# Performance work log

Measured on AMD Instinct MI355X. Metric: run time of the kernel, lower is better.

The kernel has to match this reference:

```python
import jax, jax.numpy as jnp
import numpy as np
import math

B, H, N, D = 32, 8, 257, 64  # batch, heads, seq (256 patches + 1), head dim
DIM = H * D
PIX = 256  # 16*16 flattened mask pixels
EPS = 1e-5


def setup_inputs() -> dict:
    key = jax.random.key(0)
    k1, k2, k3 = jax.random.split(key, 3)
    x = jax.random.normal(k1, (B, N, DIM), dtype=jnp.float32)
    msk = jax.random.randint(k2, (B, 16, 16), 0, 128, dtype=jnp.int32)
    W_qkv = jax.random.normal(k3, (3 * DIM, DIM), dtype=jnp.float32) * (DIM ** -0.5)
    # past_kv initialized to identity per head (np.eye tiled in the torch forward)
    past_kv = jnp.broadcast_to(jnp.eye(D, dtype=jnp.float32), (B, H, D, D))
    gn_weight = jnp.ones((H,), dtype=jnp.float32)
    gn_bias = jnp.zeros((H,), dtype=jnp.float32)
    return {"x": x, "msk": msk, "W_qkv": W_qkv, "past_kv": past_kv,
            "gn_weight": gn_weight, "gn_bias": gn_bias}


def _build_mask(msk):
    # msk: [B,16,16] int; zeros replaced by pseudo-random ints in [1,128)
    noise = jax.random.randint(jax.random.key(42), msk.shape, 1, 128, dtype=jnp.int32)
    m = jnp.where(msk == 0, noise, msk).astype(jnp.float32)
    pix = m.reshape(B, PIX, 1)                       # [B,256,1]
    ip = pix @ jnp.swapaxes(pix, 1, 2)               # [B,256,256] outer product
    ip = ip / jnp.max(ip, axis=(1, 2), keepdims=True)
    dec0 = jnp.exp(-5.0 * jnp.linspace(0.0, 1.0, PIX))       # row [256]
    t = jnp.concatenate([jnp.broadcast_to(dec0[None, None, :], (B, 1, PIX)), ip], axis=1)  # [B,257,256]
    dec1 = jnp.exp(-5.0 * jnp.linspace(0.0, 1.0, N))         # col [257]
    t = jnp.concatenate([jnp.broadcast_to(dec1[None, :, None], (B, N, 1)), t], axis=2)     # [B,257,257]
    eye = jnp.eye(N, dtype=bool)
    t = jnp.where(eye, 1.0, t)   # fill_diagonal_(1)
    t = jnp.tril(t)
    return t[:, None, :, :]      # [B,1,N,N] broadcast over heads


def reference(x, msk, W_qkv, past_kv, gn_weight, gn_bias):
    scale = D ** -0.5  # decay_mask == chunk_decay == inner_decay == dim_heads**-0.5
    qkv = x @ W_qkv.T                                # [B,N,3*DIM]
    q, k, v = jnp.split(qkv, 3, axis=-1)
    def heads(t):
        return t.reshape(B, N, H, D).transpose(0, 2, 1, 3)  # b n (h d) -> b h n d
    q, k, v = heads(q), heads(k), heads(v)

    retention = jnp.einsum('bhnd,bhmd->bhnm', q, k) * scale
    weights_before = jax.nn.softmax(retention / math.sqrt(D), axis=-1)

    mask = _build_mask(msk)
    retention = retention * mask
    weights_after = jax.nn.softmax(retention / math.sqrt(D), axis=-1)

    inner_retention = jnp.einsum('bhnm,bhmd->bhnd', retention, v)
    cross_retention = jnp.einsum('bhnd,bhde->bhne', q, past_kv) * scale
    r = inner_retention + cross_retention            # [B,H,N,D]

    # GroupNorm(groups=H, channels=H): normalize each head over (N,D)
    mean = jnp.mean(r, axis=(2, 3), keepdims=True)
    var = jnp.mean((r - mean) ** 2, axis=(2, 3), keepdims=True)
    rn = (r - mean) / jnp.sqrt(var + EPS)
    rn = rn * gn_weight[None, :, None, None] + gn_bias[None, :, None, None]

    output = rn.transpose(0, 2, 1, 3).reshape(B, N, H * D)  # b h n d -> b n (h d)
    return (output, weights_before, weights_after)
```

## Files before the change

### kernel.cpp

```cpp
#include <hip/hip_runtime.h>
#include <stdint.h>

#define WB_OFF   4210688ull
#define WA_OFF   21119232ull

typedef short short8 __attribute__((ext_vector_type(8)));
typedef float floatx4 __attribute__((ext_vector_type(4)));
typedef __attribute__((address_space(1))) const unsigned int gu32;
typedef __attribute__((address_space(3))) unsigned int lu32;

__device__ __forceinline__ unsigned short f2bf(float f){
  union { float f; uint32_t u; } v; v.f = f;
  uint32_t u = v.u;
  uint32_t r = (u + 0x7FFFu + ((u >> 16) & 1u)) >> 16;
  return (unsigned short)r;
}

__device__ __forceinline__ void threefry(uint32_t k0, uint32_t k1, uint32_t c0, uint32_t c1,
                                         uint32_t& o0, uint32_t& o1){
  const uint32_t ks2 = k0 ^ k1 ^ 0x1BD11BDAu;
  uint32_t x0 = c0 + k0, x1 = c1 + k1;
#define TF_R4(a,b,c,d) \
  x0+=x1; x1=(x1<<(a))|(x1>>(32-(a))); x1^=x0; \
  x0+=x1; x1=(x1<<(b))|(x1>>(32-(b))); x1^=x0; \
  x0+=x1; x1=(x1<<(c))|(x1>>(32-(c))); x1^=x0; \
  x0+=x1; x1=(x1<<(d))|(x1>>(32-(d))); x1^=x0;
  TF_R4(13,15,26,6)  x0+=k1;  x1+=ks2+1u;
  TF_R4(17,29,16,24) x0+=ks2; x1+=k0+2u;
  TF_R4(13,15,26,6)  x0+=k0;  x1+=k1+3u;
  TF_R4(17,29,16,24) x0+=k1;  x1+=ks2+4u;
  TF_R4(13,15,26,6)  x0+=ks2; x1+=k0+5u;
#undef TF_R4
  o0 = x0; o1 = x1;
}

__global__ __launch_bounds__(256) void prep_kernel(const int* __restrict__ msk,
                                                   float* __restrict__ mnorm){
  const int b = blockIdx.x, p = threadIdx.x;
  const int i = b*256 + p;
  uint32_t A0, A1, B0, B1;
  threefry(0u, 42u, 0u, 0u, A0, A1);
  threefry(0u, 42u, 0u, 1u, B0, B1);
  uint32_t h0, h1, l0, l1;
  threefry(A0, A1, 0u, (uint32_t)i, h0, h1);
  threefry(B0, B1, 0u, (uint32_t)i, l0, l1);
  uint32_t hb = h0 ^ h1, lb = l0 ^ l1;
  uint32_t off = ((hb % 127u) * 16u + (lb % 127u)) % 127u;
  int mv = msk[i];
  float m = (mv == 0) ? (float)(1u + off) : (float)mv;
  __shared__ float sm[256];
  sm[p] = m; __syncthreads();
  for (int s = 128; s > 0; s >>= 1){
    if (p < s) sm[p] = fmaxf(sm[p], sm[p+s]);
    __syncthreads();
  }
  mnorm[i] = m / sm[0];
}

__global__ __launch_bounds__(256) void cvt_kernel(const float* __restrict__ x,
                                                  const float* __restrict__ w,
                                                  unsigned short* __restrict__ xb,
                                                  unsigned short* __restrict__ wb){
  int i = blockIdx.x*256 + threadIdx.x;
  if (i < 1052672){
    float4 v = ((const float4*)x)[i];
    ushort4 o; o.x=f2bf(v.x); o.y=f2bf(v.y); o.z=f2bf(v.z); o.w=f2bf(v.w);
    ((ushort4*)xb)[i] = o;
  } else if (i < 1249280){
    int j = i - 1052672;
    float4 v = ((const float4*)w)[j];
    ushort4 o; o.x=f2bf(v.x); o.y=f2bf(v.y); o.z=f2bf(v.z); o.w=f2bf(v.w);
    ((ushort4*)wb)[j] = o;
  }
}

__global__ __launch_bounds__(256) void qkv_gemm(const unsigned short* __restrict__ xb,
                                                const unsigned short* __restrict__ wb,
                                                unsigned short* __restrict__ qkv){
  __shared__ unsigned short sm2[128*64*2 + 128*8];
  unsigned short* al = sm2;
  unsigned short* bl = sm2 + 128*64;
  unsigned short* c_lds = sm2;
  const int bn = blockIdx.x, bm = blockIdx.y;
  const int tid = threadIdx.x;
  const int wave = tid >> 6, lane = tid & 63;
  const int l16 = lane & 15, lq = lane >> 4;
  const int wm = (wave & 1) * 64, wn = (wave >> 1) * 64;
  const int row0 = tid >> 3;
  const int ccg = ((tid & 7) ^ (row0 & 7)) * 8;
  const int sx = (l16 & 7);
  floatx4 acc[4][4] = {};
  for (int kk = 0; kk < 512; kk += 64){
    #pragma unroll
    for (int p = 0; p < 4; p++){
      int row = p*32 + row0;
      int gm = bm*128 + row; if (gm > 8223) gm = 8223;
      __builtin_amdgcn_global_load_lds((gu32*)&xb[(size_t)gm*512 + kk + ccg],
                                       (lu32*)&al[row*64 + (tid & 7)*8], 16, 0, 0);
      int gn = bn*128 + row;
      __builtin_amdgcn_global_load_lds((gu32*)&wb[(size_t)gn*512 + kk + ccg],
                                       (lu32*)&bl[row*64 + (tid & 7)*8], 16, 0, 0);
    }
    __syncthreads();
    #pragma unroll
    for (int ks = 0; ks < 2; ks++){
      short8 af[4], bf4[4];
      #pragma unroll
      for (int mi = 0; mi < 4; mi++){
        int ch = (ks*4 + lq) ^ sx;
        af[mi] = *(const short8*)&al[(wm + mi*16 + l16)*64 + ch*8];
      }
      #pragma unroll
      for (int ni = 0; ni < 4; ni++){
        int ch = (ks*4 + lq) ^ sx;
        bf4[ni] = *(const short8*)&bl[(wn + ni*16 + l16)*64 + ch*8];
      }
      #pragma unroll
      for (int mi = 0; mi < 4; mi++)
        #pragma unroll
        for (int ni = 0; ni < 4; ni++)
          acc[mi][ni] = __builtin_amdgcn_mfma_f32_16x16x32_bf16(af[mi], bf4[ni], acc[mi][ni], 0, 0, 0);
    }
    __syncthreads();
  }
  #pragma unroll
  for (int mi = 0; mi < 4; mi++)
    #pragma unroll
    for (int ni = 0; ni < 4; ni++)
      #pragma unroll
      for (int r = 0; r < 4; r++)
        c_lds[(wm + mi*16 + lq*4 + r)*136 + wn + ni*16 + l16] = f2bf(acc[mi][ni][r]);
  __syncthreads();
  for (int i = tid; i < 128*16; i += 256){
    int row = i >> 4, cc = (i & 15)*8;
    int gm = bm*128 + row;
    if (gm < 8224){
      ushort4 v0 = *(const ushort4*)&c_lds[row*136 + cc];
      ushort4 v1 = *(const ushort4*)&c_lds[row*136 + cc + 4];
      *(ushort4*)&qkv[(size_t)gm*1536 + bn*128 + cc] = v0;
      *(ushort4*)&qkv[(size_t)gm*1536 + bn*128 + cc + 4] = v1;
    }
  }
}

__global__ __launch_bounds__(256, 3) void retention_kernel(
    const unsigned short* __restrict__ qkv,
    const float* __restrict__ past_kv,
    const float* __restrict__ mnorm,
    float* __restrict__ out,
    float* __restrict__ partials){
  const int t  = blockIdx.x;
  const int bh = blockIdx.y;
  const int b = bh >> 3, h = bh & 7;
  const int tid = threadIdx.x;
  const int wave = tid >> 6, lane = tid & 63;
  const int l16 = lane & 15, lq = lane >> 4;
  const int rw = wave * 16;

  extern __shared__ unsigned char smem[];
  unsigned short* kl  = (unsigned short*)smem;
  unsigned short* vT  = (unsigned short*)smem;
  float* bufw         = (float*)(smem + wave*8224);
  unsigned short* pkl = (unsigned short*)(smem + 39168);
  unsigned short* plw = (unsigned short*)(smem + 39168 + wave*1280);
  float* mn  = (float*)(smem + 48384);
  float* red = (float*)(smem + 49408);

  {
    uint32_t* z = (uint32_t*)(kl + 257*72);
    for (int i = tid; i < 540; i += 256) z[i] = 0;
  }
  for (int c = tid; c < 257*16; c += 256){
    int row = c >> 4, c4 = (c & 15) * 4;
    ushort4 v = *(const ushort4*)&qkv[(size_t)(b*257 + row)*1536 + 512 + h*64 + c4];
    *(ushort4*)&kl[row*72 + c4] = v;
  }
  for (int c = tid; c < 64*16; c += 256){
    int d = c >> 4, e4 = (c & 15) * 4;
    float4 v = *(const float4*)&past_kv[(size_t)bh*4096 + d*64 + e4];
    pkl[(e4+0)*72 + d] = f2bf(0.125f * v.x);
    pkl[(e4+1)*72 + d] = f2bf(0.125f * v.y);
    pkl[(e4+2)*72 + d] = f2bf(0.125f * v.z);
    pkl[(e4+3)*72 + d] = f2bf(0.125f * v.w);
  }
  mn[tid] = mnorm[b*256 + tid];
  int giA = t*64 + rw + l16; if (giA > 256) giA = 256;
  short8 aq[2];
  aq[0] = *(const short8*)&qkv[(size_t)(b*257 + giA)*1536 + h*64 + lq*8];
  aq[1] = *(const short8*)&qkv[(size_t)(b*257 + giA)*1536 + h*64 + 32 + lq*8];
  __syncthreads();

  floatx4 acc2[4] = {};
  #pragma unroll
  for (int ks = 0; ks < 2; ks++)
    #pragma unroll
    for (int ni = 0; ni < 4; ni++){
      short8 bb = *(const short8*)&pkl[(ni*16 + l16)*72 + ks*32 + lq*8];
      acc2[ni] = __builtin_amdgcn_mfma_f32_16x16x32_bf16(aq[ks], bb, acc2[ni], 0, 0, 0);
    }

  floatx4 acc[17] = {};
  #pragma unroll
  for (int ks = 0; ks < 2; ks++)
    #pragma unroll
    for (int c = 0; c < 17; c++){
      short8 bb = *(const short8*)&kl[(c*16 + l16)*72 + ks*32 + lq*8];
      acc[c] = __builtin_amdgcn_mfma_f32_16x16x32_bf16(aq[ks], bb, acc[c], 0, 0, 0);
    }
  #pragma unroll
  for (int c = 0; c < 17; c++) acc[c] *= 0.125f;

  __syncthreads();

  int gi[4]; bool rowok[4];
  #pragma unroll
  for (int r = 0; r < 4; r++){ gi[r] = t*64 + rw + lq*4 + r; rowok[r] = (gi[r] < 257); }

  float mx[4], sum_[4], inv_[4];

  #pragma unroll
  for (int r = 0; r < 4; r++) mx[r] = -3.0e38f;
  #pragma unroll
  for (int c = 0; c < 17; c++){
    bool jok = (c < 16) || (l16 == 0);
    if (jok){
      #pragma unroll
      for (int r = 0; r < 4; r++) mx[r] = fmaxf(mx[r], acc[c][r]);
    }
  }
  #pragma unroll
  for (int m = 1; m < 16; m <<= 1)
    #pragma unroll
    for (int r = 0; r < 4; r++) mx[r] = fmaxf(mx[r], __shfl_xor(mx[r], m, 64));
  #pragma unroll
  for (int r = 0; r < 4; r++) sum_[r] = 0.f;
  #pragma unroll
  for (int c = 0; c < 17; c++){
    bool jok = (c < 16) || (l16 == 0);
    if (jok){
      #pragma unroll
      for (int r = 0; r < 4; r++) sum_[r] += __expf((acc[c][r] - mx[r]) * 0.125f);
    }
  }
  #pragma unroll
  for (int m = 1; m < 16; m <<= 1)
    #pragma unroll
    for (int r = 0; r < 4; r++) sum_[r] += __shfl_xor(sum_[r], m, 64);
  #pragma unroll
  for (int r = 0; r < 4; r++) inv_[r] = 1.0f / sum_[r];

  #pragma unroll
  for (int hh = 0; hh < 2; hh++){
    if ((lq >> 1) == hh){
      int lr0 = lq*4 - hh*8;
      #pragma unroll
      for (int c = 0; c < 17; c++){
        int j = c*16 + l16;
        if (j < 257){
          #pragma unroll
          for (int r = 0; r < 4; r++)
            bufw[(lr0 + r)*257 + j] = __expf((acc[c][r] - mx[r]) * 0.125f) * inv_[r];
        }
      }
    }
    int row0 = t*64 + rw + hh*8;
    int nrow = 257 - row0; if (nrow < 0) nrow = 0; if (nrow > 8) nrow = 8;
    int n = nrow * 257;
    if (n > 0){
      size_t gb = WB_OFF + (size_t)bh*66049 + (size_t)row0*257;
      int o0 = (int)((4 - (gb & 3)) & 3);
      if (lane < o0 && lane < n) out[gb + lane] = bufw[lane];
      for (int base = o0 + lane*4; base < n; base += 256){
        if (base + 3 < n){
          float4 v; v.x = bufw[base]; v.y = bufw[base+1]; v.z = bufw[base+2]; v.w = bufw[base+3];
          *(float4*)&out[gb + base] = v;
        } else {
          #pragma unroll
          for (int e = 0; e < 4; e++) if (base + e < n) out[gb + base + e] = bufw[base + e];
        }
      }
    }
  }

  #pragma unroll
  for (int c = 0; c < 17; c++){
    int j = c*16 + l16;
    #pragma unroll
    for (int r = 0; r < 4; r++){
      int ii = gi[r] > 256 ? 256 : gi[r];
      float mv;
      if (j > ii)       mv = 0.f;
      else if (j == ii) mv = 1.f;
      else if (j == 0)  mv = __expf(-5.f * (float)ii * (1.f/256.f));
      else              mv = mn[ii-1] * mn[j-1];
      acc[c][r] *= mv;
    }
  }

  #pragma unroll
  for (int r = 0; r < 4; r++) mx[r] = -3.0e38f;
  #pragma unroll
  for (int c = 0; c < 17; c++){
    bool jok = (c < 16) || (l16 == 0);
    if (jok){
      #pragma unroll
      for (int r = 0; r < 4; r++) mx[r] = fmaxf(mx[r], acc[c][r]);
    }
  }
  #pragma unroll
  for (int m = 1; m < 16; m <<= 1)
    #pragma unroll
    for (int r = 0; r < 4; r++) mx[r] = fmaxf(mx[r], __shfl_xor(mx[r], m, 64));
  #pragma unroll
  for (int r = 0; r < 4; r++) sum_[r] = 0.f;
  #pragma unroll
  for (int c = 0; c < 17; c++){
    bool jok = (c < 16) || (l16 == 0);
    if (jok){
      #pragma unroll
      for (int r = 0; r < 4; r++) sum_[r] += __expf((acc[c][r] - mx[r]) * 0.125f);
    }
  }
  #pragma unroll
  for (int m = 1; m < 16; m <<= 1)
    #pragma unroll
    for (int r = 0; r < 4; r++) sum_[r] += __shfl_xor(sum_[r], m, 64);
  #pragma unroll
  for (int r = 0; r < 4; r++) inv_[r] = 1.0f / sum_[r];

  #pragma unroll
  for (int hh = 0; hh < 2; hh++){
    if ((lq >> 1) == hh){
      int lr0 = lq*4 - hh*8;
      #pragma unroll
      for (int c = 0; c < 17; c++){
        int j = c*16 + l16;
        if (j < 257){
          #pragma unroll
          for (int r = 0; r < 4; r++)
            bufw[(lr0 + r)*257 + j] = __expf((acc[c][r] - mx[r]) * 0.125f) * inv_[r];
        }
      }
    }
    int row0 = t*64 + rw + hh*8;
    int nrow = 257 - row0; if (nrow < 0) nrow = 0; if (nrow > 8) nrow = 8;
    int n = nrow * 257;
    if (n > 0){
      size_t gb = WA_OFF + (size_t)bh*66049 + (size_t)row0*257;
      int o0 = (int)((4 - (gb & 3)) & 3);
      if (lane < o0 && lane < n) out[gb + lane] = bufw[lane];
      for (int base = o0 + lane*4; base < n; base += 256){
        if (base + 3 < n){
          float4 v; v.x = bufw[base]; v.y = bufw[base+1]; v.z = bufw[base+2]; v.w = bufw[base+3];
          *(float4*)&out[gb + base] = v;
        } else {
          #pragma unroll
          for (int e = 0; e < 4; e++) if (base + e < n) out[gb + base + e] = bufw[base + e];
        }
      }
    }
  }
  __syncthreads();

  for (int i = tid; i < 64*19; i += 256){
    int row = i / 19, cc = (i % 19)*2 + 258;
    *(uint32_t*)&vT[row*296 + cc] = 0;
  }
  if (tid < 64) vT[tid*296 + 257] = 0;
  for (int c = tid; c < 257*16; c += 256){
    int row = c >> 4, c4 = (c & 15) * 4;
    ushort4 v = *(const ushort4*)&qkv[(size_t)(b*257 + row)*1536 + 1024 + h*64 + c4];
    vT[(c4+0)*296 + row] = v.x;
    vT[(c4+1)*296 + row] = v.y;
    vT[(c4+2)*296 + row] = v.z;
    vT[(c4+3)*296 + row] = v.w;
  }
  __syncthreads();

  const int nks = (t == 4) ? 9 : (2*t + 2);
  for (int ks = 0; ks < nks; ks++){
    #pragma unroll
    for (int cc = 0; cc < 2; cc++){
      int f = ks*2 + cc;
      #pragma unroll
      for (int r = 0; r < 4; r++){
        float val = (f < 17 && (f*16 + l16) < 257) ? acc[f][r] : 0.f;
        plw[(lq*4 + r)*40 + cc*16 + l16] = f2bf(val);
      }
    }
    short8 a = *(const short8*)&plw[l16*40 + lq*8];
    #pragma unroll
    for (int ni = 0; ni < 4; ni++){
      short8 bb = *(const short8*)&vT[(ni*16 + l16)*296 + ks*32 + lq*8];
      acc2[ni] = __builtin_amdgcn_mfma_f32_16x16x32_bf16(a, bb, acc2[ni], 0, 0, 0);
    }
  }

  float ls = 0.f, lss = 0.f;
  #pragma unroll
  for (int ni = 0; ni < 4; ni++)
    #pragma unroll
    for (int r = 0; r < 4; r++)
      if (rowok[r]){
        float v = acc2[ni][r];
        ls += v; lss += v*v;
        out[(size_t)(b*257 + gi[r])*512 + h*64 + ni*16 + l16] = v;
      }
  #pragma unroll
  for (int m = 1; m < 64; m <<= 1){ ls += __shfl_xor(ls, m, 64); lss += __shfl_xor(lss, m, 64); }
  if (lane == 0){ red[wave*2] = ls; red[wave*2 + 1] = lss; }
  __syncthreads();
  if (tid == 0){
    partials[((size_t)bh*5 + t)*2 + 0] = red[0] + red[2] + red[4] + red[6];
    partials[((size_t)bh*5 + t)*2 + 1] = red[1] + red[3] + red[5] + red[7];
  }
}

__global__ __launch_bounds__(256) void norm_kernel(const float* __restrict__ partials,
                                                   const float* __restrict__ gnw,
                                                   const float* __restrict__ gnb,
                                                   float* __restrict__ out){
  const int bh = blockIdx.x, b = bh >> 3, h = bh & 7;
  float s = 0.f, s2 = 0.f;
  #pragma unroll
  for (int tt = 0; tt < 5; tt++){
    s  += partials[(bh*5 + tt)*2 + 0];
    s2 += partials[(bh*5 + tt)*2 + 1];
  }
  const float cnt = 257.f * 64.f;
  float mean = s / cnt;
  float var  = s2 / cnt - mean * mean;
  float isd  = rsqrtf(var + 1e-5f);
  float wsc  = gnw[h] * isd;
  float bia  = gnb[h] - mean * wsc;
  for (int idx = threadIdx.x; idx < 257*16; idx += 256){
    int n = idx >> 4, e4 = (idx & 15) * 4;
    size_t off = (size_t)(b*257 + n)*512 + h*64 + e4;
    float4 v = *(float4*)&out[off];
    v.x = v.x * wsc + bia; v.y = v.y * wsc + bia;
    v.z = v.z * wsc + bia; v.w = v.w * wsc + bia;
    *(float4*)&out[off] = v;
  }
}

extern "C" void kernel_launch(void* const* d_in, const int* in_sizes, int n_in,
                              void* d_out, int out_size, void* d_ws, size_t ws_size,
                              hipStream_t stream){
  (void)in_sizes; (void)n_in; (void)out_size; (void)ws_size;
  const float* x   = (const float*)d_in[0];
  const int*   msk = (const int*)d_in[1];
  const float* w   = (const float*)d_in[2];
  const float* pkv = (const float*)d_in[3];
  const float* gnw = (const float*)d_in[4];
  const float* gnb = (const float*)d_in[5];
  float* out = (float*)d_out;

  unsigned short* qkv = (unsigned short*)d_ws;
  unsigned short* xb  = (unsigned short*)((char*)d_ws + 25264128);
  unsigned short* wb  = (unsigned short*)((char*)d_ws + 33685504);
  float* mnorm    = (float*)((char*)d_ws + 35258368);
  float* partials = (float*)((char*)d_ws + 35291136);

  hipLaunchKernelGGL(prep_kernel, dim3(32), dim3(256), 0, stream, msk, mnorm);
  hipLaunchKernelGGL(cvt_kernel, dim3(4880), dim3(256), 0, stream, x, w, xb, wb);
  hipLaunchKernelGGL(qkv_gemm, dim3(12, 65), dim3(256), 0, stream, xb, wb, qkv);
  hipLaunchKernelGGL(retention_kernel, dim3(5, 256), dim3(256), 49440, stream,
                     qkv, pkv, mnorm, out, partials);
  hipLaunchKernelGGL(norm_kernel, dim3(256), dim3(256), 0, stream, partials, gnw, gnb, out);
}
```

Measured before the change: 317.0 us.

## Prefetch K/V into registers, write softmax weights directly, unroll PV loop

K, V and past_kv tiles are now loaded into registers all at once before being written to shared memory, so the global loads overlap instead of running one after another. V is held in registers across the softmax phases, which removes the later global reload. The softmax weight matrices are now written straight from the accumulators with nontemporal stores instead of going through a shared-memory staging buffer, which drops one barrier. The PV loop is fully unrolled so acc[] can be indexed statically. This raises register pressure considerably (about 70 extra VGPRs under launch_bounds 256,3), risks spills, and the direct stores are scalar and less coalesced.

```diff
diff --git a/kernel.cpp b/kernel.cpp
--- a/kernel.cpp
+++ b/kernel.cpp
@@ -160,7 +160,6 @@
   extern __shared__ unsigned char smem[];
   unsigned short* kl  = (unsigned short*)smem;
   unsigned short* vT  = (unsigned short*)smem;
-  float* bufw         = (float*)(smem + wave*8224);
   unsigned short* pkl = (unsigned short*)(smem + 39168);
   unsigned short* plw = (unsigned short*)(smem + 39168 + wave*1280);
   float* mn  = (float*)(smem + 48384);
@@ -170,25 +169,56 @@
     uint32_t* z = (uint32_t*)(kl + 257*72);
     for (int i = tid; i < 540; i += 256) z[i] = 0;
   }
-  for (int c = tid; c < 257*16; c += 256){
-    int row = c >> 4, c4 = (c & 15) * 4;
-    ushort4 v = *(const ushort4*)&qkv[(size_t)(b*257 + row)*1536 + 512 + h*64 + c4];
-    *(ushort4*)&kl[row*72 + c4] = v;
-  }
-  for (int c = tid; c < 64*16; c += 256){
+  ushort4 kreg[17];
+  #pragma unroll
+  for (int u = 0; u < 17; u++){
+    int c = tid + u*256;
+    if (c < 4112){
+      int row = c >> 4, c4 = (c & 15) * 4;
+      kreg[u] = *(const ushort4*)&qkv[(size_t)(b*257 + row)*1536 + 512 + h*64 + c4];
+    }
+  }
+  float4 preg[4];
+  #pragma unroll
+  for (int u = 0; u < 4; u++){
+    int c = tid + u*256;
     int d = c >> 4, e4 = (c & 15) * 4;
-    float4 v = *(const float4*)&past_kv[(size_t)bh*4096 + d*64 + e4];
-    pkl[(e4+0)*72 + d] = f2bf(0.125f * v.x);
-    pkl[(e4+1)*72 + d] = f2bf(0.125f * v.y);
-    pkl[(e4+2)*72 + d] = f2bf(0.125f * v.z);
-    pkl[(e4+3)*72 + d] = f2bf(0.125f * v.w);
-  }
-  mn[tid] = mnorm[b*256 + tid];
+    preg[u] = *(const float4*)&past_kv[(size_t)bh*4096 + d*64 + e4];
+  }
+  float mnv = mnorm[b*256 + tid];
   int giA = t*64 + rw + l16; if (giA > 256) giA = 256;
   short8 aq[2];
   aq[0] = *(const short8*)&qkv[(size_t)(b*257 + giA)*1536 + h*64 + lq*8];
   aq[1] = *(const short8*)&qkv[(size_t)(b*257 + giA)*1536 + h*64 + 32 + lq*8];
-  __syncthreads();
+  ushort4 vreg[17];
+  #pragma unroll
+  for (int u = 0; u < 17; u++){
+    int c = tid + u*256;
+    if (c < 4112){
+      int row = c >> 4, c4 = (c & 15) * 4;
+      vreg[u] = *(const ushort4*)&qkv[(size_t)(b*257 + row)*1536 + 1024 + h*64 + c4];
+    }
+  }
+  #pragma unroll
+  for (int u = 0; u < 17; u++){
+    int c = tid + u*256;
+    if (c < 4112){
+      int row = c >> 4, c4 = (c & 15) * 4;
+      *(ushort4*)&kl[row*72 + c4] = kreg[u];
+    }
+  }
+  #pragma unroll
+  for (int u = 0; u < 4; u++){
+    int c = tid + u*256;
+    int d = c >> 4, e4 = (c & 15) * 4;
+    pkl[(e4+0)*72 + d] = f2bf(0.125f * preg[u].x);
+    pkl[(e4+1)*72 + d] = f2bf(0.125f * preg[u].y);
+    pkl[(e4+2)*72 + d] = f2bf(0.125f * preg[u].z);
+    pkl[(e4+3)*72 + d] = f2bf(0.125f * preg[u].w);
+  }
+  mn[tid] = mnv;
+  asm volatile("s_waitcnt lgkmcnt(0)" ::: "memory");
+  __builtin_amdgcn_s_barrier();
 
   floatx4 acc2[4] = {};
   #pragma unroll
@@ -210,8 +240,6 @@
   #pragma unroll
   for (int c = 0; c < 17; c++) acc[c] *= 0.125f;
 
-  __syncthreads();
-
   int gi[4]; bool rowok[4];
   #pragma unroll
   for (int r = 0; r < 4; r++){ gi[r] = t*64 + rw + lq*4 + r; rowok[r] = (gi[r] < 257); }
@@ -249,34 +277,17 @@
   #pragma unroll
   for (int r = 0; r < 4; r++) inv_[r] = 1.0f / sum_[r];
 
-  #pragma unroll
-  for (int hh = 0; hh < 2; hh++){
-    if ((lq >> 1) == hh){
-      int lr0 = lq*4 - hh*8;
+  {
+    const size_t gbase = WB_OFF + (size_t)bh*66049;
+    #pragma unroll
+    for (int r = 0; r < 4; r++){
+      size_t rb = gbase + (size_t)gi[r]*257;
       #pragma unroll
       for (int c = 0; c < 17; c++){
         int j = c*16 + l16;
-        if (j < 257){
-          #pragma unroll
-          for (int r = 0; r < 4; r++)
-            bufw[(lr0 + r)*257 + j] = __expf((acc[c][r] - mx[r]) * 0.125f) * inv_[r];
-        }
-      }
-    }
-    int row0 = t*64 + rw + hh*8;
-    int nrow = 257 - row0; if (nrow < 0) nrow = 0; if (nrow > 8) nrow = 8;
-    int n = nrow * 257;
-    if (n > 0){
-      size_t gb = WB_OFF + (size_t)bh*66049 + (size_t)row0*257;
-      int o0 = (int)((4 - (gb & 3)) & 3);
-      if (lane < o0 && lane < n) out[gb + lane] = bufw[lane];
-      for (int base = o0 + lane*4; base < n; base += 256){
-        if (base + 3 < n){
-          float4 v; v.x = bufw[base]; v.y = bufw[base+1]; v.z = bufw[base+2]; v.w = bufw[base+3];
-          *(float4*)&out[gb + base] = v;
-        } else {
-          #pragma unroll
-          for (int e = 0; e < 4; e++) if (base + e < n) out[gb + base + e] = bufw[base + e];
+        if (rowok[r] && j < 257){
+          float v = __expf((acc[c][r] - mx[r]) * 0.125f) * inv_[r];
+          __builtin_nontemporal_store(v, &out[rb + j]);
         }
       }
     }
@@ -328,34 +339,17 @@
   #pragma unroll
   for (int r = 0; r < 4; r++) inv_[r] = 1.0f / sum_[r];
 
-  #pragma unroll
-  for (int hh = 0; hh < 2; hh++){
-    if ((lq >> 1) == hh){
-      int lr0 = lq*4 - hh*8;
+  {
+    const size_t gbase = WA_OFF + (size_t)bh*66049;
+    #pragma unroll
+    for (int r = 0; r < 4; r++){
+      size_t rb = gbase + (size_t)gi[r]*257;
       #pragma unroll
       for (int c = 0; c < 17; c++){
         int j = c*16 + l16;
-        if (j < 257){
-          #pragma unroll
-          for (int r = 0; r < 4; r++)
-            bufw[(lr0 + r)*257 + j] = __expf((acc[c][r] - mx[r]) * 0.125f) * inv_[r];
-        }
-      }
-    }
-    int row0 = t*64 + rw + hh*8;
-    int nrow = 257 - row0; if (nrow < 0) nrow = 0; if (nrow > 8) nrow = 8;
-    int n = nrow * 257;
-    if (n > 0){
-      size_t gb = WA_OFF + (size_t)bh*66049 + (size_t)row0*257;
-      int o0 = (int)((4 - (gb & 3)) & 3);
-      if (lane < o0 && lane < n) out[gb + lane] = bufw[lane];
-      for (int base = o0 + lane*4; base < n; base += 256){
-        if (base + 3 < n){
-          float4 v; v.x = bufw[base]; v.y = bufw[base+1]; v.z = bufw[base+2]; v.w = bufw[base+3];
-          *(float4*)&out[gb + base] = v;
-        } else {
-          #pragma unroll
-          for (int e = 0; e < 4; e++) if (base + e < n) out[gb + base + e] = bufw[base + e];
+        if (rowok[r] && j < 257){
+          float v = __expf((acc[c][r] - mx[r]) * 0.125f) * inv_[r];
+          __builtin_nontemporal_store(v, &out[rb + j]);
         }
       }
     }
@@ -367,32 +361,38 @@
     *(uint32_t*)&vT[row*296 + cc] = 0;
   }
   if (tid < 64) vT[tid*296 + 257] = 0;
-  for (int c = tid; c < 257*16; c += 256){
-    int row = c >> 4, c4 = (c & 15) * 4;
-    ushort4 v = *(const ushort4*)&qkv[(size_t)(b*257 + row)*1536 + 1024 + h*64 + c4];
-    vT[(c4+0)*296 + row] = v.x;
-    vT[(c4+1)*296 + row] = v.y;
-    vT[(c4+2)*296 + row] = v.z;
-    vT[(c4+3)*296 + row] = v.w;
+  #pragma unroll
+  for (int u = 0; u < 17; u++){
+    int c = tid + u*256;
+    if (c < 4112){
+      int row = c >> 4, c4 = (c & 15) * 4;
+      vT[(c4+0)*296 + row] = vreg[u].x;
+      vT[(c4+1)*296 + row] = vreg[u].y;
+      vT[(c4+2)*296 + row] = vreg[u].z;
+      vT[(c4+3)*296 + row] = vreg[u].w;
+    }
   }
   __syncthreads();
 
   const int nks = (t == 4) ? 9 : (2*t + 2);
-  for (int ks = 0; ks < nks; ks++){
-    #pragma unroll
-    for (int cc = 0; cc < 2; cc++){
-      int f = ks*2 + cc;
-      #pragma unroll
-      for (int r = 0; r < 4; r++){
-        float val = (f < 17 && (f*16 + l16) < 257) ? acc[f][r] : 0.f;
-        plw[(lq*4 + r)*40 + cc*16 + l16] = f2bf(val);
-      }
-    }
-    short8 a = *(const short8*)&plw[l16*40 + lq*8];
-    #pragma unroll
-    for (int ni = 0; ni < 4; ni++){
-      short8 bb = *(const short8*)&vT[(ni*16 + l16)*296 + ks*32 + lq*8];
-      acc2[ni] = __builtin_amdgcn_mfma_f32_16x16x32_bf16(a, bb, acc2[ni], 0, 0, 0);
+  #pragma unroll
+  for (int ks = 0; ks < 9; ks++){
+    if (ks < nks){
+      #pragma unroll
+      for (int cc = 0; cc < 2; cc++){
+        const int f = ks*2 + cc;
+        #pragma unroll
+        for (int r = 0; r < 4; r++){
+          float val = (f < 17 && (f*16 + l16) < 257) ? acc[f][r] : 0.f;
+          plw[(lq*4 + r)*40 + cc*16 + l16] = f2bf(val);
+        }
+      }
+      short8 a = *(const short8*)&plw[l16*40 + lq*8];
+      #pragma unroll
+      for (int ni = 0; ni < 4; ni++){
+        short8 bb = *(const short8*)&vT[(ni*16 + l16)*296 + ks*32 + lq*8];
+        acc2[ni] = __builtin_amdgcn_mfma_f32_16x16x32_bf16(a, bb, acc2[ni], 0, 0, 0);
+      }
     }
   }
 
```

New measurement: 300.3 us. 1.06x faster.
